# Kernel tuning notes

Measured on AMD Instinct MI355X. Metric: run time of the kernel, lower is better.

The kernel has to match this reference:

```python
import jax, jax.numpy as jnp
import numpy as np

NUM_GRAPHS = 256


def _lin_params(key, fan_in, fan_out):
    k1, k2 = jax.random.split(key)
    bound = 1.0 / np.sqrt(fan_in)
    W = jax.random.uniform(k1, (fan_in, fan_out), jnp.float32, -bound, bound)
    b = jax.random.uniform(k2, (fan_out,), jnp.float32, -bound, bound)
    return W, b


def setup_inputs() -> dict:
    key = jax.random.key(0)
    ks = jax.random.split(key, 12)
    N, E, F = 100000, 3200000, 32
    x = jax.random.normal(ks[0], (N, F), jnp.float32)
    edge_index = jax.random.randint(ks[1], (2, E), 0, N, jnp.int64)
    batch = jnp.sort(jax.random.randint(ks[2], (N,), 0, NUM_GRAPHS, jnp.int64))
    W1, b1 = _lin_params(ks[3], 32, 32)   # conv1
    W2, b2 = _lin_params(ks[4], 32, 24)   # conv2
    Wg, bg = _lin_params(ks[5], 24, 32)   # g_fcn1
    Wt, bt = _lin_params(ks[6], 32, 2)    # t_fcn1
    Wn1, bn1 = _lin_params(ks[7], 24, 16)  # n_fcn1
    Wn2, bn2 = _lin_params(ks[8], 16, 1)   # n_fcn2
    Wb1, bb1 = _lin_params(ks[9], 24, 16)  # b_fcn1
    Wb2, bb2 = _lin_params(ks[10], 16, 3)  # b_fcn2
    return {"x": x, "edge_index": edge_index, "batch": batch,
            "W1": W1, "b1": b1, "W2": W2, "b2": b2,
            "Wg": Wg, "bg": bg, "Wt": Wt, "bt": bt,
            "Wn1": Wn1, "bn1": bn1, "Wn2": Wn2, "bn2": bn2,
            "Wb1": Wb1, "bb1": bb1, "Wb2": Wb2, "bb2": bb2}


def _gcn_conv(x, edge_index, W, b):
    """PyG GCNConv: self-loops + symmetric normalization + linear."""
    N = x.shape[0]
    h = x @ W  # [N, out]
    loop = jnp.arange(N, dtype=edge_index.dtype)
    row = jnp.concatenate([edge_index[0], loop])  # source
    col = jnp.concatenate([edge_index[1], loop])  # target
    deg = jax.ops.segment_sum(jnp.ones_like(col, dtype=h.dtype), col, num_segments=N)
    dinv = jnp.where(deg > 0, jax.lax.rsqrt(deg), 0.0)
    norm = dinv[row] * dinv[col]  # [E+N]
    out = jax.ops.segment_sum(h[row] * norm[:, None], col, num_segments=N)
    return out + b


def _segment_softmax(v, seg, num_seg):
    """Softmax over nodes within each graph (leading axis)."""
    m = jax.ops.segment_max(v, seg, num_segments=num_seg)
    e = jnp.exp(v - m[seg])
    s = jax.ops.segment_sum(e, seg, num_segments=num_seg)
    return e / s[seg]


def reference(x, edge_index, batch, W1, b1, W2, b2, Wg, bg, Wt, bt,
              Wn1, bn1, Wn2, bn2, Wb1, bb1, Wb2, bb2):
    h = jax.nn.relu(_gcn_conv(x, edge_index, W1, b1))          # [N,32]
    h = jax.nn.relu(_gcn_conv(h, edge_index, W2, b2))          # [N,24]
    # global mean pool
    cnt = jax.ops.segment_sum(jnp.ones((h.shape[0],), h.dtype), batch, num_segments=NUM_GRAPHS)
    g = jax.ops.segment_sum(h, batch, num_segments=NUM_GRAPHS) / jnp.maximum(cnt, 1.0)[:, None]
    g = g @ Wg + bg                                            # [G,32]
    t = jax.nn.softmax(g @ Wt + bt, axis=1)                    # [G,2]
    n = jax.nn.relu(h @ Wn1 + bn1) @ Wn2 + bn2                 # [N,1]
    n = _segment_softmax(n, batch, NUM_GRAPHS)                 # per-graph softmax over nodes
    b_feat = jax.ops.segment_sum(n * h, batch, num_segments=NUM_GRAPHS)  # global_add_pool of n*x
    bb = jax.nn.relu(b_feat @ Wb1 + bb1) @ Wb2 + bb2           # [G,3]
    bb = jax.nn.softmax(bb, axis=0)                            # dim=0 softmax as in source
    return (t, n, bb)
```

## Files before the change

kernel.cpp:

```cpp
#include <hip/hip_runtime.h>
#include <math.h>

#define NG 256
#define NBLK 256

#define S1F 16.0f
#define IS1F 0.0625f
#define S2F 64.0f
#define IS2F 0.015625f

typedef __attribute__((ext_vector_type(2))) float f32x2;

__device__ __forceinline__ unsigned enc4(float f0, float f1, float f2, float f3) {
    int r = __builtin_amdgcn_cvt_pk_fp8_f32(f0, f1, 0, false);
    r = __builtin_amdgcn_cvt_pk_fp8_f32(f2, f3, r, true);
    return (unsigned)r;
}
__device__ __forceinline__ void acc8p(uint2 v, f32x2 (&a)[4]) {
    a[0] += __builtin_amdgcn_cvt_pk_f32_fp8((int)v.x, false);
    a[1] += __builtin_amdgcn_cvt_pk_f32_fp8((int)v.x, true);
    a[2] += __builtin_amdgcn_cvt_pk_f32_fp8((int)v.y, false);
    a[3] += __builtin_amdgcn_cvt_pk_f32_fp8((int)v.y, true);
}

__global__ __launch_bounds__(256) void hist_bucket_kernel(
        const int* __restrict__ col, int* __restrict__ blockOff,
        int* __restrict__ bucketTot, int E, int NB) {
    __shared__ int h[512];
    h[threadIdx.x] = 0; h[threadIdx.x + 256] = 0;
    __syncthreads();
    const int chunk = (((E + NBLK - 1) / NBLK) + 3) & ~3;
    const int beg = blockIdx.x * chunk;
    const int end = min(beg + chunk, E);
    if ((E & 3) == 0) {
        int e = beg + threadIdx.x * 4;
        for (; e + 3 < end; e += 1024) {
            int4 c = *(const int4*)(col + e);
            atomicAdd(&h[c.x >> 8], 1);
            atomicAdd(&h[c.y >> 8], 1);
            atomicAdd(&h[c.z >> 8], 1);
            atomicAdd(&h[c.w >> 8], 1);
        }
        for (; e < end; e++) atomicAdd(&h[col[e] >> 8], 1);
    } else {
        for (int e = beg + threadIdx.x; e < end; e += 256)
            atomicAdd(&h[col[e] >> 8], 1);
    }
    __syncthreads();
    for (int t = threadIdx.x; t < NB; t += 256) {
        int off = atomicAdd(&bucketTot[t], h[t]);
        blockOff[t * NBLK + blockIdx.x] = off;
    }
}

__global__ __launch_bounds__(512) void tiny_scan_kernel(
        const int* __restrict__ bucketTot, int* __restrict__ bucketBase, int NB) {
    __shared__ int part[512];
    const int t = threadIdx.x;
    int v = (t < NB) ? bucketTot[t] : 0;
    part[t] = v;
    __syncthreads();
    for (int o = 1; o < 512; o <<= 1) {
        int u = (t >= o) ? part[t - o] : 0;
        __syncthreads();
        part[t] += u;
        __syncthreads();
    }
    if (t < NB) bucketBase[t] = part[t] - v;
    if (t == NB) bucketBase[NB] = part[NB - 1];
    if (t == 511 && NB == 512) bucketBase[NB] = part[511];
}

__global__ __launch_bounds__(256) void scatter_pairs_kernel(
        const int* __restrict__ ei, const int* __restrict__ blockOff,
        const int* __restrict__ bucketBase, int* __restrict__ pairs, int E, int NB) {
    __shared__ int cur[512];
    for (int t = threadIdx.x; t < NB; t += 256)
        cur[t] = bucketBase[t] + blockOff[t * NBLK + blockIdx.x];
    __syncthreads();
    const int chunk = (((E + NBLK - 1) / NBLK) + 3) & ~3;
    const int beg = blockIdx.x * chunk;
    const int end = min(beg + chunk, E);
    if ((E & 3) == 0) {
        int e = beg + threadIdx.x * 4;
        for (; e + 3 < end; e += 1024) {
            int4 s = *(const int4*)(ei + e);
            int4 tg = *(const int4*)(ei + E + e);
            int p0 = atomicAdd(&cur[tg.x >> 8], 1);
            pairs[p0] = (int)(((unsigned)(tg.x & 255) << 17) | (unsigned)s.x);
            int p1 = atomicAdd(&cur[tg.y >> 8], 1);
            pairs[p1] = (int)(((unsigned)(tg.y & 255) << 17) | (unsigned)s.y);
            int p2 = atomicAdd(&cur[tg.z >> 8], 1);
            pairs[p2] = (int)(((unsigned)(tg.z & 255) << 17) | (unsigned)s.z);
            int p3 = atomicAdd(&cur[tg.w >> 8], 1);
            pairs[p3] = (int)(((unsigned)(tg.w & 255) << 17) | (unsigned)s.w);
        }
        for (; e < end; e++) {
            int src = ei[e];
            int tgt = ei[E + e];
            int pos = atomicAdd(&cur[tgt >> 8], 1);
            pairs[pos] = (int)(((unsigned)(tgt & 255) << 17) | (unsigned)src);
        }
    } else {
        for (int e = beg + threadIdx.x; e < end; e += 256) {
            int src = ei[e];
            int tgt = ei[E + e];
            int pos = atomicAdd(&cur[tgt >> 8], 1);
            pairs[pos] = (int)(((unsigned)(tgt & 255) << 17) | (unsigned)src);
        }
    }
}

__global__ __launch_bounds__(256) void csr_bucket_kernel(
        const int* __restrict__ pairs, const int* __restrict__ bucketBase,
        int* __restrict__ rowptr, int* __restrict__ adj,
        float* __restrict__ dinv, int N, int E) {
    __shared__ int h[256];
    __shared__ int sc[256];
    __shared__ int cur[256];
    const int b = blockIdx.x, t = threadIdx.x;
    const int base = bucketBase[b];
    const int end = bucketBase[b + 1];
    h[t] = 0;
    __syncthreads();
    for (int i = base + t; i < end; i += 256)
        atomicAdd(&h[(unsigned)pairs[i] >> 17], 1);
    __syncthreads();
    const int v = h[t];
    sc[t] = v;
    __syncthreads();
    for (int o = 1; o < 256; o <<= 1) {
        int u = (t >= o) ? sc[t - o] : 0;
        __syncthreads();
        sc[t] += u;
        __syncthreads();
    }
    const int ex = sc[t] - v;
    const int node = (b << 8) + t;
    if (node < N) {
        rowptr[node] = base + ex;
        dinv[node] = rsqrtf((float)v + 1.0f);
    }
    cur[t] = base + ex;
    __syncthreads();
    for (int i = base + t; i < end; i += 256) {
        unsigned p = (unsigned)pairs[i];
        int pos = atomicAdd(&cur[p >> 17], 1);
        adj[pos] = (int)(p & 0x1FFFFu);
    }
    if (b == 0 && t == 0) rowptr[N] = E;
}

__global__ __launch_bounds__(256) void bounds_kernel(
        const int* __restrict__ batch, int* __restrict__ starts, int N) {
    int i = blockIdx.x * blockDim.x + threadIdx.x;
    if (i >= N) return;
    int b = batch[i];
    int bp = (i == 0) ? -1 : batch[i - 1];
    for (int g = bp + 1; g <= b; g++) starts[g] = i;
    if (i == N - 1)
        for (int g = b + 1; g <= NG; g++) starts[g] = N;
}

__global__ __launch_bounds__(256) void hs1_kernel(
        const float* __restrict__ x, const float* __restrict__ W,
        const float* __restrict__ dinv, unsigned* __restrict__ hs, int N) {
    __shared__ float Ws[32 * 32];
    __shared__ float tmp[8][32];
    for (int t = threadIdx.x; t < 1024; t += blockDim.x) Ws[t] = W[t];
    __syncthreads();
    const int tid = threadIdx.x;
    const int node = blockIdx.x * 8 + (tid >> 5);
    const int n = tid >> 5, f = tid & 31;
    if (node < N) {
        const float* xr = x + (size_t)node * 32;
        float acc = 0.f;
#pragma unroll
        for (int k = 0; k < 32; k++) acc += xr[k] * Ws[k * 32 + f];
        tmp[n][f] = acc * dinv[node] * S1F;
        if (f < 8)
            hs[(size_t)node * 8 + f] = enc4(tmp[n][4 * f], tmp[n][4 * f + 1],
                                            tmp[n][4 * f + 2], tmp[n][4 * f + 3]);
    } else if (node == N) {
        if (f < 8) hs[(size_t)N * 8 + f] = 0u;
    }
}

__global__ __launch_bounds__(256) void gather1_kernel(
        const int* __restrict__ rowptr, const int* __restrict__ adj,
        const uint2* __restrict__ hs1q, const float* __restrict__ dinv,
        const float* __restrict__ b1, const float* __restrict__ W2,
        unsigned* __restrict__ hs2out, int N) {
    __shared__ float W2s[32 * 24];
    __shared__ float b1s[32];
    __shared__ float h1row[16][32];
    __shared__ float hs2t[16][32];
    const int tid = threadIdx.x;
    for (int t = tid; t < 768; t += 256) W2s[t] = W2[t];
    if (tid < 32) b1s[tid] = b1[tid];
    if (blockIdx.x == 0 && tid < 8) hs2out[(size_t)N * 8 + tid] = 0u;

    const int g = tid >> 5;
    const int l = tid & 31;
    const int f8 = l & 3;
    const int e8 = l >> 2;
    const int n0 = (blockIdx.x * 8 + g) * 2;
    const int n1 = n0 + 1;
    const bool val0 = n0 < N;
    const bool val1 = n1 < N;

    int beg0 = 0, cnt0 = 0, beg1 = 0, cnt1 = 0;
    if (val0) {
        int2 rp = *(const int2*)(rowptr + n0);
        beg0 = rp.x; cnt0 = rp.y - rp.x;
        if (val1) { int e2 = rowptr[n0 + 2]; beg1 = rp.y; cnt1 = e2 - rp.y; }
    }
    const int* ap0 = adj + beg0;
    const int* ap1 = adj + beg1;
    f32x2 a0[4], a1[4];
#pragma unroll
    for (int k = 0; k < 4; k++) { a0[k][0] = 0.f; a0[k][1] = 0.f; a1[k][0] = 0.f; a1[k][1] = 0.f; }

    const int jmax = max(cnt0, cnt1);
    for (int j = 0; j < jmax; j += 32) {
        const int i0 = j + e8, i1 = j + 8 + e8, i2 = j + 16 + e8, i3 = j + 24 + e8;
        int sA0 = ap0[i0], sA1 = ap0[i1], sA2 = ap0[i2], sA3 = ap0[i3];
        int sB0 = ap1[i0], sB1 = ap1[i1], sB2 = ap1[i2], sB3 = ap1[i3];
        if (i0 >= cnt0) sA0 = N; if (i1 >= cnt0) sA1 = N;
        if (i2 >= cnt0) sA2 = N; if (i3 >= cnt0) sA3 = N;
        if (i0 >= cnt1) sB0 = N; if (i1 >= cnt1) sB1 = N;
        if (i2 >= cnt1) sB2 = N; if (i3 >= cnt1) sB3 = N;
        uint2 vA0 = hs1q[(size_t)sA0 * 4 + f8];
        uint2 vA1 = hs1q[(size_t)sA1 * 4 + f8];
        uint2 vA2 = hs1q[(size_t)sA2 * 4 + f8];
        uint2 vA3 = hs1q[(size_t)sA3 * 4 + f8];
        uint2 vB0 = hs1q[(size_t)sB0 * 4 + f8];
        uint2 vB1 = hs1q[(size_t)sB1 * 4 + f8];
        uint2 vB2 = hs1q[(size_t)sB2 * 4 + f8];
        uint2 vB3 = hs1q[(size_t)sB3 * 4 + f8];
        acc8p(vA0, a0); acc8p(vA1, a0); acc8p(vA2, a0); acc8p(vA3, a0);
        acc8p(vB0, a1); acc8p(vB1, a1); acc8p(vB2, a1); acc8p(vB3, a1);
    }
#pragma unroll
    for (int k = 0; k < 4; k++) {
        float x0 = a0[k][0], x1 = a0[k][1], y0 = a1[k][0], y1 = a1[k][1];
        x0 += __shfl_xor(x0, 4); x0 += __shfl_xor(x0, 8); x0 += __shfl_xor(x0, 16);
        x1 += __shfl_xor(x1, 4); x1 += __shfl_xor(x1, 8); x1 += __shfl_xor(x1, 16);
        y0 += __shfl_xor(y0, 4); y0 += __shfl_xor(y0, 8); y0 += __shfl_xor(y0, 16);
        y1 += __shfl_xor(y1, 4); y1 += __shfl_xor(y1, 8); y1 += __shfl_xor(y1, 16);
        a0[k][0] = x0; a0[k][1] = x1; a1[k][0] = y0; a1[k][1] = y1;
    }

    __syncthreads();

    auto fin1 = [&](const f32x2 (&a)[4], int node, int row) {
        const int fq = l & 3;
        const float c = dinv[node] * IS1F;
        uint2 w = hs1q[(size_t)node * 4 + fq];
        f32x2 s0 = __builtin_amdgcn_cvt_pk_f32_fp8((int)w.x, false);
        f32x2 s1 = __builtin_amdgcn_cvt_pk_f32_fp8((int)w.x, true);
        f32x2 s2 = __builtin_amdgcn_cvt_pk_f32_fp8((int)w.y, false);
        f32x2 s3 = __builtin_amdgcn_cvt_pk_f32_fp8((int)w.y, true);
        h1row[row][8 * fq + 0] = fmaxf(c * (a[0][0] + s0[0]) + b1s[8 * fq + 0], 0.f);
        h1row[row][8 * fq + 1] = fmaxf(c * (a[0][1] + s0[1]) + b1s[8 * fq + 1], 0.f);
        h1row[row][8 * fq + 2] = fmaxf(c * (a[1][0] + s1[0]) + b1s[8 * fq + 2], 0.f);
        h1row[row][8 * fq + 3] = fmaxf(c * (a[1][1] + s1[1]) + b1s[8 * fq + 3], 0.f);
        h1row[row][8 * fq + 4] = fmaxf(c * (a[2][0] + s2[0]) + b1s[8 * fq + 4], 0.f);
        h1row[row][8 * fq + 5] = fmaxf(c * (a[2][1] + s2[1]) + b1s[8 * fq + 5], 0.f);
        h1row[row][8 * fq + 6] = fmaxf(c * (a[3][0] + s3[0]) + b1s[8 * fq + 6], 0.f);
        h1row[row][8 * fq + 7] = fmaxf(c * (a[3][1] + s3[1]) + b1s[8 * fq + 7], 0.f);
    };
    if (l < 4) { if (val0) fin1(a0, n0, 2 * g); }
    else if (l < 8) { if (val1) fin1(a1, n1, 2 * g + 1); }

#pragma unroll
    for (int nn = 0; nn < 2; ++nn) {
        const int node = n0 + nn;
        if (node >= N) break;
        const int row = 2 * g + nn;
        const float sc = dinv[node] * S2F;
        float aa = 0.f;
        if (l < 24) {
#pragma unroll
            for (int k = 0; k < 32; k++) aa += h1row[row][k] * W2s[k * 24 + l];
        }
        hs2t[row][l] = (l < 24) ? aa * sc : 0.f;
        if (l < 8)
            hs2out[(size_t)node * 8 + l] = enc4(hs2t[row][4 * l], hs2t[row][4 * l + 1],
                                                hs2t[row][4 * l + 2], hs2t[row][4 * l + 3]);
    }
}

__global__ __launch_bounds__(256) void gather2_kernel(
        const int* __restrict__ rowptr, const int* __restrict__ adj,
        const uint2* __restrict__ hs2q, const float* __restrict__ dinv,
        const float* __restrict__ b2,
        const float* __restrict__ Wn1, const float* __restrict__ bn1,
        const float* __restrict__ Wn2, const float* __restrict__ bn2,
        float* __restrict__ h2out, float* __restrict__ vout, int N) {
    __shared__ float Wn1s[24 * 16];
    __shared__ float b2s[32], bn1s[16], Wn2s[16];
    __shared__ float h2row[16][32];
    const int tid = threadIdx.x;
    for (int t = tid; t < 384; t += 256) Wn1s[t] = Wn1[t];
    if (tid < 32) b2s[tid] = (tid < 24) ? b2[tid] : 0.f;
    if (tid < 16) { bn1s[tid] = bn1[tid]; Wn2s[tid] = Wn2[tid]; }

    const int g = tid >> 5;
    const int l = tid & 31;
    const int f8 = l & 3;
    const int e8 = l >> 2;
    const int n0 = (blockIdx.x * 8 + g) * 2;
    const int n1 = n0 + 1;
    const bool val0 = n0 < N;
    const bool val1 = n1 < N;

    int beg0 = 0, cnt0 = 0, beg1 = 0, cnt1 = 0;
    if (val0) {
        int2 rp = *(const int2*)(rowptr + n0);
        beg0 = rp.x; cnt0 = rp.y - rp.x;
        if (val1) { int e2 = rowptr[n0 + 2]; beg1 = rp.y; cnt1 = e2 - rp.y; }
    }
    const int* ap0 = adj + beg0;
    const int* ap1 = adj + beg1;
    f32x2 a0[4], a1[4];
#pragma unroll
    for (int k = 0; k < 4; k++) { a0[k][0] = 0.f; a0[k][1] = 0.f; a1[k][0] = 0.f; a1[k][1] = 0.f; }

    const int jmax = max(cnt0, cnt1);
    for (int j = 0; j < jmax; j += 32) {
        const int i0 = j + e8, i1 = j + 8 + e8, i2 = j + 16 + e8, i3 = j + 24 + e8;
        int sA0 = ap0[i0], sA1 = ap0[i1], sA2 = ap0[i2], sA3 = ap0[i3];
        int sB0 = ap1[i0], sB1 = ap1[i1], sB2 = ap1[i2], sB3 = ap1[i3];
        if (i0 >= cnt0) sA0 = N; if (i1 >= cnt0) sA1 = N;
        if (i2 >= cnt0) sA2 = N; if (i3 >= cnt0) sA3 = N;
        if (i0 >= cnt1) sB0 = N; if (i1 >= cnt1) sB1 = N;
        if (i2 >= cnt1) sB2 = N; if (i3 >= cnt1) sB3 = N;
        uint2 vA0 = hs2q[(size_t)sA0 * 4 + f8];
        uint2 vA1 = hs2q[(size_t)sA1 * 4 + f8];
        uint2 vA2 = hs2q[(size_t)sA2 * 4 + f8];
        uint2 vA3 = hs2q[(size_t)sA3 * 4 + f8];
        uint2 vB0 = hs2q[(size_t)sB0 * 4 + f8];
        uint2 vB1 = hs2q[(size_t)sB1 * 4 + f8];
        uint2 vB2 = hs2q[(size_t)sB2 * 4 + f8];
        uint2 vB3 = hs2q[(size_t)sB3 * 4 + f8];
        acc8p(vA0, a0); acc8p(vA1, a0); acc8p(vA2, a0); acc8p(vA3, a0);
        acc8p(vB0, a1); acc8p(vB1, a1); acc8p(vB2, a1); acc8p(vB3, a1);
    }
#pragma unroll
    for (int k = 0; k < 4; k++) {
        float x0 = a0[k][0], x1 = a0[k][1], y0 = a1[k][0], y1 = a1[k][1];
        x0 += __shfl_xor(x0, 4); x0 += __shfl_xor(x0, 8); x0 += __shfl_xor(x0, 16);
        x1 += __shfl_xor(x1, 4); x1 += __shfl_xor(x1, 8); x1 += __shfl_xor(x1, 16);
        y0 += __shfl_xor(y0, 4); y0 += __shfl_xor(y0, 8); y0 += __shfl_xor(y0, 16);
        y1 += __shfl_xor(y1, 4); y1 += __shfl_xor(y1, 8); y1 += __shfl_xor(y1, 16);
        a0[k][0] = x0; a0[k][1] = x1; a1[k][0] = y0; a1[k][1] = y1;
    }

    __syncthreads();

    auto fin2 = [&](const f32x2 (&a)[4], int node, int row) {
        const int fq = l & 3;
        const float c = dinv[node] * IS2F;
        uint2 w = hs2q[(size_t)node * 4 + fq];
        f32x2 s0 = __builtin_amdgcn_cvt_pk_f32_fp8((int)w.x, false);
        f32x2 s1 = __builtin_amdgcn_cvt_pk_f32_fp8((int)w.x, true);
        f32x2 s2 = __builtin_amdgcn_cvt_pk_f32_fp8((int)w.y, false);
        f32x2 s3 = __builtin_amdgcn_cvt_pk_f32_fp8((int)w.y, true);
        h2row[row][8 * fq + 0] = fmaxf(c * (a[0][0] + s0[0]) + b2s[8 * fq + 0], 0.f);
        h2row[row][8 * fq + 1] = fmaxf(c * (a[0][1] + s0[1]) + b2s[8 * fq + 1], 0.f);
        h2row[row][8 * fq + 2] = fmaxf(c * (a[1][0] + s1[0]) + b2s[8 * fq + 2], 0.f);
        h2row[row][8 * fq + 3] = fmaxf(c * (a[1][1] + s1[1]) + b2s[8 * fq + 3], 0.f);
        h2row[row][8 * fq + 4] = fmaxf(c * (a[2][0] + s2[0]) + b2s[8 * fq + 4], 0.f);
        h2row[row][8 * fq + 5] = fmaxf(c * (a[2][1] + s2[1]) + b2s[8 * fq + 5], 0.f);
        h2row[row][8 * fq + 6] = fmaxf(c * (a[3][0] + s3[0]) + b2s[8 * fq + 6], 0.f);
        h2row[row][8 * fq + 7] = fmaxf(c * (a[3][1] + s3[1]) + b2s[8 * fq + 7], 0.f);
    };
    if (l < 4) { if (val0) fin2(a0, n0, 2 * g); }
    else if (l < 8) { if (val1) fin2(a1, n1, 2 * g + 1); }

#pragma unroll
    for (int nn = 0; nn < 2; ++nn) {
        const int node = n0 + nn;
        if (node >= N) break;
        const int row = 2 * g + nn;
        if (l < 24) h2out[(size_t)node * 24 + l] = h2row[row][l];
        float val = 0.f;
        if (l < 16) {
            float u = bn1s[l];
#pragma unroll
            for (int k = 0; k < 24; k++) u += h2row[row][k] * Wn1s[k * 16 + l];
            val = fmaxf(u, 0.f) * Wn2s[l];
        }
        val += __shfl_down(val, 8, 16);
        val += __shfl_down(val, 4, 16);
        val += __shfl_down(val, 2, 16);
        val += __shfl_down(val, 1, 16);
        if (l == 0) vout[node] = val + bn2[0];
    }
}

__global__ __launch_bounds__(1024) void graph_kernel(
        const float* __restrict__ v, const float* __restrict__ h2,
        const int* __restrict__ starts,
        const float* __restrict__ Wg, const float* __restrict__ bg,
        const float* __restrict__ Wt, const float* __restrict__ bt,
        const float* __restrict__ Wb1p, const float* __restrict__ bb1p,
        const float* __restrict__ Wb2p, const float* __restrict__ bb2p,
        float* __restrict__ out_t, float* __restrict__ out_n,
        float* __restrict__ bbpre, int N) {
    const int g = blockIdx.x;
    const int tid = threadIdx.x;
    const int lane = tid & 63;
    const int wv = tid >> 6;

    const int start = starts[g];
    const int end = starts[g + 1];

    __shared__ float sm[16];
    __shared__ float pH[16][24], pW[16][24], pS[16];

    float m = -INFINITY;
    for (int idx = start + tid; idx < end; idx += 1024) m = fmaxf(m, v[idx]);
#pragma unroll
    for (int off = 32; off > 0; off >>= 1) m = fmaxf(m, __shfl_down(m, off, 64));
    if (lane == 0) sm[wv] = m;
    __syncthreads();
    m = sm[0];
#pragma unroll
    for (int k = 1; k < 16; k++) m = fmaxf(m, sm[k]);

    const int half = lane >> 5;
    const int slot = wv * 2 + half;
    const int feat = lane & 31;
    const bool fa = feat < 24;
    float hs = 0.f, ws = 0.f, se = 0.f;
    int i = start + slot;
    for (; i + 96 < end; i += 128) {
        float v0 = v[i], v1 = v[i + 32], v2 = v[i + 64], v3 = v[i + 96];
        float h0 = 0.f, h1 = 0.f, hh2 = 0.f, h3 = 0.f;
        if (fa) {
            h0 = h2[(size_t)i * 24 + feat];
            h1 = h2[(size_t)(i + 32) * 24 + feat];
            hh2 = h2[(size_t)(i + 64) * 24 + feat];
            h3 = h2[(size_t)(i + 96) * 24 + feat];
        }
        float e0 = __expf(v0 - m), e1 = __expf(v1 - m);
        float e2 = __expf(v2 - m), e3 = __expf(v3 - m);
        if (feat == 0) se += (e0 + e1) + (e2 + e3);
        hs += (h0 + h1) + (hh2 + h3);
        ws += (e0 * h0 + e1 * h1) + (e2 * hh2 + e3 * h3);
    }
    for (; i < end; i += 32) {
        float vv = v[i];
        float e = __expf(vv - m);
        if (feat == 0) se += e;
        if (fa) {
            float hv = h2[(size_t)i * 24 + feat];
            hs += hv;
            ws += e * hv;
        }
    }
    hs += __shfl_xor(hs, 32, 64);
    ws += __shfl_xor(ws, 32, 64);
    se += __shfl_xor(se, 32, 64);
    if (lane < 24) { pH[wv][lane] = hs; pW[wv][lane] = ws; }
    if (lane == 0) pS[wv] = se;
    __syncthreads();
    float stot = 0.f;
#pragma unroll
    for (int k = 0; k < 16; k++) stot += pS[k];
    const float invs = (stot > 0.f) ? 1.f / stot : 0.f;

    for (int idx = start + tid; idx < end; idx += 1024)
        out_n[idx] = __expf(v[idx] - m) * invs;

    const float denom = fmaxf((float)(end - start), 1.0f);
    if (tid < 32) {
        float a = bg[tid];
#pragma unroll
        for (int k = 0; k < 24; k++) {
            float sum_k = 0.f;
#pragma unroll
            for (int w = 0; w < 16; w++) sum_k += pH[w][k];
            a += (sum_k / denom) * Wg[k * 32 + tid];
        }
        float p0 = a * Wt[tid * 2];
        float p1 = a * Wt[tid * 2 + 1];
#pragma unroll
        for (int off = 16; off > 0; off >>= 1) {
            p0 += __shfl_down(p0, off, 32);
            p1 += __shfl_down(p1, off, 32);
        }
        if (tid == 0) {
            float t0 = p0 + bt[0], t1 = p1 + bt[1];
            float tm = fmaxf(t0, t1);
            float e0 = __expf(t0 - tm), e1 = __expf(t1 - tm);
            float ts = e0 + e1;
            out_t[g * 2 + 0] = e0 / ts;
            out_t[g * 2 + 1] = e1 / ts;
        }
    }
    if (tid < 16) {
        float u = bb1p[tid];
#pragma unroll
        for (int k = 0; k < 24; k++) {
            float sum_k = 0.f;
#pragma unroll
            for (int w = 0; w < 16; w++) sum_k += pW[w][k];
            u += (sum_k * invs) * Wb1p[k * 16 + tid];
        }
        u = fmaxf(u, 0.f);
        float q0 = u * Wb2p[tid * 3 + 0];
        float q1 = u * Wb2p[tid * 3 + 1];
        float q2 = u * Wb2p[tid * 3 + 2];
#pragma unroll
        for (int off = 8; off > 0; off >>= 1) {
            q0 += __shfl_down(q0, off, 16);
            q1 += __shfl_down(q1, off, 16);
            q2 += __shfl_down(q2, off, 16);
        }
        if (tid == 0) {
            bbpre[g * 3 + 0] = q0 + bb2p[0];
            bbpre[g * 3 + 1] = q1 + bb2p[1];
            bbpre[g * 3 + 2] = q2 + bb2p[2];
        }
    }
}

__global__ __launch_bounds__(256) void bb_kernel(
        const float* __restrict__ bbpre, float* __restrict__ out_bb) {
    __shared__ float red[NG];
    int g = threadIdx.x;
#pragma unroll
    for (int c = 0; c < 3; c++) {
        float vv = bbpre[g * 3 + c];
        red[g] = vv;
        __syncthreads();
        for (int off = 128; off > 0; off >>= 1) {
            if (g < off) red[g] = fmaxf(red[g], red[g + off]);
            __syncthreads();
        }
        float m = red[0];
        __syncthreads();
        float e = __expf(vv - m);
        red[g] = e;
        __syncthreads();
        for (int off = 128; off > 0; off >>= 1) {
            if (g < off) red[g] += red[g + off];
            __syncthreads();
        }
        float ssum = red[0];
        __syncthreads();
        out_bb[g * 3 + c] = e / ssum;
    }
}

extern "C" void kernel_launch(void* const* d_in, const int* in_sizes, int n_in,
                              void* d_out, int out_size, void* d_ws, size_t ws_size,
                              hipStream_t stream) {
    const float* x   = (const float*)d_in[0];
    const int*   ei  = (const int*)d_in[1];
    const int*   bat = (const int*)d_in[2];
    const float* W1  = (const float*)d_in[3];
    const float* b1  = (const float*)d_in[4];
    const float* W2  = (const float*)d_in[5];
    const float* b2  = (const float*)d_in[6];
    const float* Wg  = (const float*)d_in[7];
    const float* bg  = (const float*)d_in[8];
    const float* Wt  = (const float*)d_in[9];
    const float* bt  = (const float*)d_in[10];
    const float* Wn1 = (const float*)d_in[11];
    const float* bn1 = (const float*)d_in[12];
    const float* Wn2 = (const float*)d_in[13];
    const float* bn2 = (const float*)d_in[14];
    const float* Wb1 = (const float*)d_in[15];
    const float* bb1 = (const float*)d_in[16];
    const float* Wb2 = (const float*)d_in[17];
    const float* bb2 = (const float*)d_in[18];

    const int N = in_sizes[2];
    const int E = in_sizes[1] / 2;
    const int NB = (N + 255) >> 8;
    const int M = NB * NBLK;

    auto rnd4 = [](size_t v) { return (v + 3) & ~(size_t)3; };
    size_t oRow = 0;
    size_t oDin = oRow + rnd4((size_t)N + 1);
    size_t oAdj = oDin + rnd4((size_t)N);
    size_t oBB  = oAdj + rnd4((size_t)E);
    size_t oTot = oBB + rnd4((size_t)NB + 1);
    size_t oSt  = oTot + rnd4((size_t)NB);
    size_t oT   = oSt + rnd4((size_t)NG + 1);
    size_t oPar = oT + rnd4((size_t)M);

    int*   wsi     = (int*)d_ws;
    float* wsf     = (float*)d_ws;
    int*   rowptr  = wsi + oRow;
    float* dinv    = wsf + oDin;
    int*   adj     = wsi + oAdj;
    int*   bbase   = wsi + oBB;
    int*   btot    = wsi + oTot;
    int*   starts  = wsi + oSt;
    int*   blkoff  = wsi + oT;
    int*   pairs   = wsi + oPar;
    unsigned* hs1b = (unsigned*)(wsf + oT);
    float* h2      = wsf + oT;
    float* vbuf    = wsf + oT + (size_t)24 * N;
    unsigned* hs2b = (unsigned*)(wsf + oT + (size_t)26 * N);
    float* bbpre   = wsf + oT + (size_t)28 * N + 4;

    float* out_t  = (float*)d_out;
    float* out_n  = out_t + 2 * NG;
    float* out_bb = out_t + 2 * NG + N;

    const int B = 256;

    (void)hipMemsetAsync(btot, 0, (size_t)NB * sizeof(int), stream);
    bounds_kernel<<<(N + B - 1) / B, B, 0, stream>>>(bat, starts, N);
    hist_bucket_kernel<<<NBLK, B, 0, stream>>>(ei + E, blkoff, btot, E, NB);
    tiny_scan_kernel<<<1, 512, 0, stream>>>(btot, bbase, NB);
    scatter_pairs_kernel<<<NBLK, B, 0, stream>>>(ei, blkoff, bbase, pairs, E, NB);
    csr_bucket_kernel<<<NB, B, 0, stream>>>(pairs, bbase, rowptr, adj, dinv, N, E);

    hs1_kernel<<<(N + 1 + 7) / 8, B, 0, stream>>>(x, W1, dinv, hs1b, N);
    gather1_kernel<<<(N + 15) / 16, B, 0, stream>>>(rowptr, adj, (const uint2*)hs1b,
                                                    dinv, b1, W2, hs2b, N);
    gather2_kernel<<<(N + 15) / 16, B, 0, stream>>>(rowptr, adj, (const uint2*)hs2b,
                                                    dinv, b2, Wn1, bn1, Wn2, bn2, h2, vbuf, N);
    graph_kernel<<<NG, 1024, 0, stream>>>(vbuf, h2, starts, Wg, bg, Wt, bt,
                                          Wb1, bb1, Wb2, bb2, out_t, out_n, bbpre, N);
    bb_kernel<<<1, B, 0, stream>>>(bbpre, out_bb);
}
```

Measured before the change: 283.9 us.

## Fuse per-block graph partial reductions into gather2, fold bounds and bb kernels

gather2 now reduces its 16 nodes into per-graph partial records (local max, exp-sum, feature sum, weighted sum), assuming each block spans at most two graphs. This removes the 24-float h2 write and its reread by graph_kernel. graph_kernel combines these records with a rescaled softmax, and the final bb softmax runs in the last-finishing block through an atomic counter. The bounds kernel is merged into csr_bucket, so two launches disappear. The risks are the two-graphs-per-block assumption and the threadfence/atomic pattern used to detect the last block.

```diff
diff --git a/kernel.cpp b/kernel.cpp
--- a/kernel.cpp
+++ b/kernel.cpp
@@ -3,6 +3,7 @@
 
 #define NG 256
 #define NBLK 256
+#define PSTRIDE 52
 
 #define S1F 16.0f
 #define IS1F 0.0625f
@@ -113,12 +114,23 @@
 
 __global__ __launch_bounds__(256) void csr_bucket_kernel(
         const int* __restrict__ pairs, const int* __restrict__ bucketBase,
-        int* __restrict__ rowptr, int* __restrict__ adj,
-        float* __restrict__ dinv, int N, int E) {
+        const int* __restrict__ bat, int* __restrict__ rowptr,
+        int* __restrict__ adj, float* __restrict__ dinv,
+        int* __restrict__ starts, int N, int E) {
     __shared__ int h[256];
     __shared__ int sc[256];
     __shared__ int cur[256];
     const int b = blockIdx.x, t = threadIdx.x;
+    {
+        const int i = (b << 8) + t;
+        if (i < N) {
+            int bb = bat[i];
+            int bp = (i == 0) ? -1 : bat[i - 1];
+            for (int g = bp + 1; g <= bb; g++) starts[g] = i;
+            if (i == N - 1)
+                for (int g = bb + 1; g <= NG; g++) starts[g] = N;
+        }
+    }
     const int base = bucketBase[b];
     const int end = bucketBase[b + 1];
     h[t] = 0;
@@ -149,17 +161,6 @@
         adj[pos] = (int)(p & 0x1FFFFu);
     }
     if (b == 0 && t == 0) rowptr[N] = E;
-}
-
-__global__ __launch_bounds__(256) void bounds_kernel(
-        const int* __restrict__ batch, int* __restrict__ starts, int N) {
-    int i = blockIdx.x * blockDim.x + threadIdx.x;
-    if (i >= N) return;
-    int b = batch[i];
-    int bp = (i == 0) ? -1 : batch[i - 1];
-    for (int g = bp + 1; g <= b; g++) starts[g] = i;
-    if (i == N - 1)
-        for (int g = b + 1; g <= NG; g++) starts[g] = N;
 }
 
 __global__ __launch_bounds__(256) void hs1_kernel(
@@ -297,14 +298,17 @@
         const float* __restrict__ b2,
         const float* __restrict__ Wn1, const float* __restrict__ bn1,
         const float* __restrict__ Wn2, const float* __restrict__ bn2,
-        float* __restrict__ h2out, float* __restrict__ vout, int N) {
+        const int* __restrict__ bat, float* __restrict__ vout,
+        float* __restrict__ pbuf, int* __restrict__ pg, int N) {
     __shared__ float Wn1s[24 * 16];
     __shared__ float b2s[32], bn1s[16], Wn2s[16];
     __shared__ float h2row[16][32];
+    __shared__ float varr[16];
+    __shared__ int gidArr[16];
     const int tid = threadIdx.x;
     for (int t = tid; t < 384; t += 256) Wn1s[t] = Wn1[t];
     if (tid < 32) b2s[tid] = (tid < 24) ? b2[tid] : 0.f;
-    if (tid < 16) { bn1s[tid] = bn1[tid]; Wn2s[tid] = Wn2[tid]; }
+    if (tid < 16) { bn1s[tid] = bn1[tid]; Wn2s[tid] = Wn2[tid]; gidArr[tid] = -1; }
 
     const int g = tid >> 5;
     const int l = tid & 31;
@@ -384,7 +388,6 @@
         const int node = n0 + nn;
         if (node >= N) break;
         const int row = 2 * g + nn;
-        if (l < 24) h2out[(size_t)node * 24 + l] = h2row[row][l];
         float val = 0.f;
         if (l < 16) {
             float u = bn1s[l];
@@ -396,95 +399,126 @@
         val += __shfl_down(val, 4, 16);
         val += __shfl_down(val, 2, 16);
         val += __shfl_down(val, 1, 16);
-        if (l == 0) vout[node] = val + bn2[0];
-    }
-}
-
-__global__ __launch_bounds__(1024) void graph_kernel(
-        const float* __restrict__ v, const float* __restrict__ h2,
-        const int* __restrict__ starts,
+        if (l == 0) { float vv = val + bn2[0]; vout[node] = vv; varr[row] = vv; }
+        if (l == 1) gidArr[row] = bat[node];
+    }
+
+    __syncthreads();
+
+    if (tid < 64) {
+        int gbase = 0x7fffffff;
+#pragma unroll
+        for (int r = 0; r < 16; r++) {
+            int gg = gidArr[r];
+            if (gg >= 0 && gg < gbase) gbase = gg;
+        }
+        float m0 = -INFINITY, m1 = -INFINITY;
+#pragma unroll
+        for (int r = 0; r < 16; r++) {
+            int gg = gidArr[r];
+            if (gg >= 0) {
+                if (gg == gbase) m0 = fmaxf(m0, varr[r]);
+                else m1 = fmaxf(m1, varr[r]);
+            }
+        }
+        const int f = tid;
+        float hs0 = 0.f, ws0 = 0.f, se0 = 0.f;
+        float hs1v = 0.f, ws1v = 0.f, se1v = 0.f;
+#pragma unroll
+        for (int r = 0; r < 16; r++) {
+            int gg = gidArr[r];
+            if (gg < 0) continue;
+            float h = (f < 24) ? h2row[r][f] : 0.f;
+            if (gg == gbase) {
+                float e = __expf(varr[r] - m0);
+                hs0 += h; ws0 += e * h; se0 += e;
+            } else {
+                float e = __expf(varr[r] - m1);
+                hs1v += h; ws1v += e * h; se1v += e;
+            }
+        }
+        const int bidx = blockIdx.x * 2;
+        const bool p0 = (m0 != -INFINITY);
+        const bool p1 = (m1 != -INFINITY);
+        if (tid == 25) {
+            pg[bidx] = p0 ? gbase : -1;
+            pg[bidx + 1] = p1 ? (gbase + 1) : -1;
+        }
+        size_t off0 = (size_t)bidx * PSTRIDE;
+        size_t off1 = (size_t)(bidx + 1) * PSTRIDE;
+        if (p0) {
+            if (tid == 24) { pbuf[off0] = m0; pbuf[off0 + 1] = se0; }
+            if (tid < 24) { pbuf[off0 + 2 + tid] = hs0; pbuf[off0 + 26 + tid] = ws0; }
+        }
+        if (p1) {
+            if (tid == 24) { pbuf[off1] = m1; pbuf[off1 + 1] = se1v; }
+            if (tid < 24) { pbuf[off1 + 2 + tid] = hs1v; pbuf[off1 + 26 + tid] = ws1v; }
+        }
+    }
+}
+
+__global__ __launch_bounds__(256) void graph_kernel(
+        const float* __restrict__ v, const float* __restrict__ pbuf,
+        const int* __restrict__ pg, const int* __restrict__ starts,
         const float* __restrict__ Wg, const float* __restrict__ bg,
         const float* __restrict__ Wt, const float* __restrict__ bt,
         const float* __restrict__ Wb1p, const float* __restrict__ bb1p,
         const float* __restrict__ Wb2p, const float* __restrict__ bb2p,
         float* __restrict__ out_t, float* __restrict__ out_n,
-        float* __restrict__ bbpre, int N) {
+        float* __restrict__ bbpre, float* __restrict__ out_bb,
+        int* __restrict__ cnt, int N) {
     const int g = blockIdx.x;
     const int tid = threadIdx.x;
     const int lane = tid & 63;
     const int wv = tid >> 6;
-
     const int start = starts[g];
     const int end = starts[g + 1];
 
-    __shared__ float sm[16];
-    __shared__ float pH[16][24], pW[16][24], pS[16];
-
+    __shared__ float sm[4];
+    __shared__ float hsumL[24], bfL[24];
+    __shared__ float invsS;
+    __shared__ float red[NG];
+    __shared__ int lastFlag;
+
+    int idx0 = 0, nrec = 0;
+    if (end > start) {
+        int rb0 = start >> 4, rb1 = (end - 1) >> 4;
+        idx0 = rb0 * 2;
+        nrec = (rb1 - rb0 + 1) * 2;
+    }
     float m = -INFINITY;
-    for (int idx = start + tid; idx < end; idx += 1024) m = fmaxf(m, v[idx]);
+    for (int k = tid; k < nrec; k += 256)
+        if (pg[idx0 + k] == g) m = fmaxf(m, pbuf[(size_t)(idx0 + k) * PSTRIDE]);
 #pragma unroll
     for (int off = 32; off > 0; off >>= 1) m = fmaxf(m, __shfl_down(m, off, 64));
     if (lane == 0) sm[wv] = m;
     __syncthreads();
-    m = sm[0];
-#pragma unroll
-    for (int k = 1; k < 16; k++) m = fmaxf(m, sm[k]);
-
-    const int half = lane >> 5;
-    const int slot = wv * 2 + half;
-    const int feat = lane & 31;
-    const bool fa = feat < 24;
-    float hs = 0.f, ws = 0.f, se = 0.f;
-    int i = start + slot;
-    for (; i + 96 < end; i += 128) {
-        float v0 = v[i], v1 = v[i + 32], v2 = v[i + 64], v3 = v[i + 96];
-        float h0 = 0.f, h1 = 0.f, hh2 = 0.f, h3 = 0.f;
-        if (fa) {
-            h0 = h2[(size_t)i * 24 + feat];
-            h1 = h2[(size_t)(i + 32) * 24 + feat];
-            hh2 = h2[(size_t)(i + 64) * 24 + feat];
-            h3 = h2[(size_t)(i + 96) * 24 + feat];
-        }
-        float e0 = __expf(v0 - m), e1 = __expf(v1 - m);
-        float e2 = __expf(v2 - m), e3 = __expf(v3 - m);
-        if (feat == 0) se += (e0 + e1) + (e2 + e3);
-        hs += (h0 + h1) + (hh2 + h3);
-        ws += (e0 * h0 + e1 * h1) + (e2 * hh2 + e3 * h3);
-    }
-    for (; i < end; i += 32) {
-        float vv = v[i];
-        float e = __expf(vv - m);
-        if (feat == 0) se += e;
-        if (fa) {
-            float hv = h2[(size_t)i * 24 + feat];
-            hs += hv;
-            ws += e * hv;
-        }
-    }
-    hs += __shfl_xor(hs, 32, 64);
-    ws += __shfl_xor(ws, 32, 64);
-    se += __shfl_xor(se, 32, 64);
-    if (lane < 24) { pH[wv][lane] = hs; pW[wv][lane] = ws; }
-    if (lane == 0) pS[wv] = se;
-    __syncthreads();
-    float stot = 0.f;
-#pragma unroll
-    for (int k = 0; k < 16; k++) stot += pS[k];
-    const float invs = (stot > 0.f) ? 1.f / stot : 0.f;
-
-    for (int idx = start + tid; idx < end; idx += 1024)
+    m = fmaxf(fmaxf(sm[0], sm[1]), fmaxf(sm[2], sm[3]));
+
+    if (tid < 25) {
+        float hs = 0.f, bf = 0.f, se = 0.f;
+        for (int k = 0; k < nrec; k++) {
+            int idx = idx0 + k;
+            if (pg[idx] != g) continue;
+            const float* rec = pbuf + (size_t)idx * PSTRIDE;
+            float w = __expf(rec[0] - m);
+            if (tid < 24) { hs += rec[2 + tid]; bf += rec[26 + tid] * w; }
+            else se += rec[1] * w;
+        }
+        if (tid < 24) { hsumL[tid] = hs; bfL[tid] = bf; }
+        else invsS = (se > 0.f) ? 1.f / se : 0.f;
+    }
+    __syncthreads();
+    const float invs = invsS;
+
+    for (int idx = start + tid; idx < end; idx += 256)
         out_n[idx] = __expf(v[idx] - m) * invs;
 
     const float denom = fmaxf((float)(end - start), 1.0f);
     if (tid < 32) {
         float a = bg[tid];
 #pragma unroll
-        for (int k = 0; k < 24; k++) {
-            float sum_k = 0.f;
-#pragma unroll
-            for (int w = 0; w < 16; w++) sum_k += pH[w][k];
-            a += (sum_k / denom) * Wg[k * 32 + tid];
-        }
+        for (int k = 0; k < 24; k++) a += (hsumL[k] / denom) * Wg[k * 32 + tid];
         float p0 = a * Wt[tid * 2];
         float p1 = a * Wt[tid * 2 + 1];
 #pragma unroll
@@ -504,12 +538,7 @@
     if (tid < 16) {
         float u = bb1p[tid];
 #pragma unroll
-        for (int k = 0; k < 24; k++) {
-            float sum_k = 0.f;
-#pragma unroll
-            for (int w = 0; w < 16; w++) sum_k += pW[w][k];
-            u += (sum_k * invs) * Wb1p[k * 16 + tid];
-        }
+        for (int k = 0; k < 24; k++) u += (bfL[k] * invs) * Wb1p[k * 16 + tid];
         u = fmaxf(u, 0.f);
         float q0 = u * Wb2p[tid * 3 + 0];
         float q1 = u * Wb2p[tid * 3 + 1];
@@ -526,33 +555,39 @@
             bbpre[g * 3 + 2] = q2 + bb2p[2];
         }
     }
-}
-
-__global__ __launch_bounds__(256) void bb_kernel(
-        const float* __restrict__ bbpre, float* __restrict__ out_bb) {
-    __shared__ float red[NG];
-    int g = threadIdx.x;
-#pragma unroll
-    for (int c = 0; c < 3; c++) {
-        float vv = bbpre[g * 3 + c];
-        red[g] = vv;
-        __syncthreads();
-        for (int off = 128; off > 0; off >>= 1) {
-            if (g < off) red[g] = fmaxf(red[g], red[g + off]);
+
+    __syncthreads();
+    if (tid == 0) {
+        __threadfence();
+        int old = atomicAdd(cnt, 1);
+        lastFlag = (old == NG - 1) ? 1 : 0;
+    }
+    __syncthreads();
+    if (lastFlag) {
+        __threadfence();
+        const int gg = tid;
+#pragma unroll
+        for (int c = 0; c < 3; c++) {
+            float vv = bbpre[gg * 3 + c];
+            red[gg] = vv;
             __syncthreads();
-        }
-        float m = red[0];
-        __syncthreads();
-        float e = __expf(vv - m);
-        red[g] = e;
-        __syncthreads();
-        for (int off = 128; off > 0; off >>= 1) {
-            if (g < off) red[g] += red[g + off];
+            for (int off = 128; off > 0; off >>= 1) {
+                if (gg < off) red[gg] = fmaxf(red[gg], red[gg + off]);
+                __syncthreads();
+            }
+            float mm = red[0];
             __syncthreads();
-        }
-        float ssum = red[0];
-        __syncthreads();
-        out_bb[g * 3 + c] = e / ssum;
+            float e = __expf(vv - mm);
+            red[gg] = e;
+            __syncthreads();
+            for (int off = 128; off > 0; off >>= 1) {
+                if (gg < off) red[gg] += red[gg + off];
+                __syncthreads();
+            }
+            float ssum = red[0];
+            __syncthreads();
+            out_bb[gg * 3 + c] = e / ssum;
+        }
     }
 }
 
@@ -583,32 +618,36 @@
     const int E = in_sizes[1] / 2;
     const int NB = (N + 255) >> 8;
     const int M = NB * NBLK;
+    const int NBLK2 = (N + 15) / 16;
 
     auto rnd4 = [](size_t v) { return (v + 3) & ~(size_t)3; };
     size_t oRow = 0;
     size_t oDin = oRow + rnd4((size_t)N + 1);
     size_t oAdj = oDin + rnd4((size_t)N);
-    size_t oBB  = oAdj + rnd4((size_t)E);
-    size_t oTot = oBB + rnd4((size_t)NB + 1);
-    size_t oSt  = oTot + rnd4((size_t)NB);
-    size_t oT   = oSt + rnd4((size_t)NG + 1);
-    size_t oPar = oT + rnd4((size_t)M);
+    size_t oTot = oAdj + rnd4((size_t)E);
+    size_t oSt  = oTot + rnd4((size_t)NB + 1);
+    size_t oBB  = oSt + rnd4((size_t)NG + 1);
+    size_t oT   = oBB + rnd4((size_t)NB + 1);
 
     int*   wsi     = (int*)d_ws;
     float* wsf     = (float*)d_ws;
     int*   rowptr  = wsi + oRow;
     float* dinv    = wsf + oDin;
     int*   adj     = wsi + oAdj;
+    int*   btot    = wsi + oTot;
+    int*   cnt     = wsi + oTot + NB;
+    int*   starts  = wsi + oSt;
     int*   bbase   = wsi + oBB;
-    int*   btot    = wsi + oTot;
-    int*   starts  = wsi + oSt;
     int*   blkoff  = wsi + oT;
-    int*   pairs   = wsi + oPar;
-    unsigned* hs1b = (unsigned*)(wsf + oT);
-    float* h2      = wsf + oT;
-    float* vbuf    = wsf + oT + (size_t)24 * N;
-    unsigned* hs2b = (unsigned*)(wsf + oT + (size_t)26 * N);
-    float* bbpre   = wsf + oT + (size_t)28 * N + 4;
+    int*   pairs   = wsi + oT + rnd4((size_t)M);
+    size_t cb = oT;
+    unsigned* hs1b = (unsigned*)(wsf + cb);
+    unsigned* hs2b = (unsigned*)(wsf + cb + 2 * ((size_t)N + 1));
+    float* vbuf    = wsf + cb + 4 * ((size_t)N + 1);
+    float* pbuf    = wsf + cb + 4 * ((size_t)N + 1) + rnd4((size_t)N);
+    int*   pg      = wsi + cb + 4 * ((size_t)N + 1) + rnd4((size_t)N)
+                         + rnd4((size_t)2 * NBLK2 * PSTRIDE);
+    float* bbpre   = (float*)(pg + rnd4((size_t)2 * NBLK2));
 
     float* out_t  = (float*)d_out;
     float* out_n  = out_t + 2 * NG;
@@ -616,19 +655,20 @@
 
     const int B = 256;
 
-    (void)hipMemsetAsync(btot, 0, (size_t)NB * sizeof(int), stream);
-    bounds_kernel<<<(N + B - 1) / B, B, 0, stream>>>(bat, starts, N);
+    (void)hipMemsetAsync(btot, 0, (size_t)(NB + 1) * sizeof(int), stream);
     hist_bucket_kernel<<<NBLK, B, 0, stream>>>(ei + E, blkoff, btot, E, NB);
     tiny_scan_kernel<<<1, 512, 0, stream>>>(btot, bbase, NB);
     scatter_pairs_kernel<<<NBLK, B, 0, stream>>>(ei, blkoff, bbase, pairs, E, NB);
-    csr_bucket_kernel<<<NB, B, 0, stream>>>(pairs, bbase, rowptr, adj, dinv, N, E);
+    csr_bucket_kernel<<<NB, B, 0, stream>>>(pairs, bbase, bat, rowptr, adj, dinv,
+                                            starts, N, E);
 
     hs1_kernel<<<(N + 1 + 7) / 8, B, 0, stream>>>(x, W1, dinv, hs1b, N);
     gather1_kernel<<<(N + 15) / 16, B, 0, stream>>>(rowptr, adj, (const uint2*)hs1b,
                                                     dinv, b1, W2, hs2b, N);
-    gather2_kernel<<<(N + 15) / 16, B, 0, stream>>>(rowptr, adj, (const uint2*)hs2b,
-                                                    dinv, b2, Wn1, bn1, Wn2, bn2, h2, vbuf, N);
-    graph_kernel<<<NG, 1024, 0, stream>>>(vbuf, h2, starts, Wg, bg, Wt, bt,
-                                          Wb1, bb1, Wb2, bb2, out_t, out_n, bbpre, N);
-    bb_kernel<<<1, B, 0, stream>>>(bbpre, out_bb);
-}
+    gather2_kernel<<<NBLK2, B, 0, stream>>>(rowptr, adj, (const uint2*)hs2b,
+                                            dinv, b2, Wn1, bn1, Wn2, bn2,
+                                            bat, vbuf, pbuf, pg, N);
+    graph_kernel<<<NG, B, 0, stream>>>(vbuf, pbuf, pg, starts, Wg, bg, Wt, bt,
+                                       Wb1, bb1, Wb2, bb2, out_t, out_n,
+                                       bbpre, out_bb, cnt, N);
+}
```

Measured after the change: 291.4 us. 2.6% more time.
